# Kernel tuning notes

Hardware: AMD Instinct MI355X
Metric: run time of the kernel (lower is better)

The kernel has to match this reference:

```python
import jax, jax.numpy as jnp
import numpy as np

B, S, H = 2, 2048, 2048
NH, NKV = 16, 4
HD = H // NH          # 128
N_REP = NH // NKV     # 4


def _rotate_half(x):
    x1, x2 = x[..., : x.shape[-1] // 2], x[..., x.shape[-1] // 2 :]
    return jnp.concatenate((-x2, x1), axis=-1)


def setup_inputs() -> dict:
    key = jax.random.key(0)
    ks = jax.random.split(key, 5)
    hidden_states = jax.random.normal(ks[0], (B, S, H), dtype=jnp.float32)
    # true rotary tables [max_seq_len, head_dim]
    inv_freq = 1.0 / (10000.0 ** (np.arange(0, HD, 2, dtype=np.float32) / HD))
    t = np.arange(S, dtype=np.float32)
    freqs = np.outer(t, inv_freq)                    # [S, HD/2]
    emb = np.concatenate([freqs, freqs], axis=-1)    # [S, HD]
    cos = jnp.asarray(np.cos(emb))
    sin = jnp.asarray(np.sin(emb))
    Wq = jax.random.normal(ks[1], (H, NH * HD), dtype=jnp.float32) * 0.02
    Wk = jax.random.normal(ks[2], (H, NKV * HD), dtype=jnp.float32) * 0.02
    Wv = jax.random.normal(ks[3], (H, NKV * HD), dtype=jnp.float32) * 0.02
    Wo = jax.random.normal(ks[4], (NH * HD, H), dtype=jnp.float32) * 0.02
    attention_mask = jnp.ones((B, S), dtype=jnp.float32)  # 1 = keep
    return {"hidden_states": hidden_states, "cos": cos, "sin": sin,
            "Wq": Wq, "Wk": Wk, "Wv": Wv, "Wo": Wo,
            "attention_mask": attention_mask}


def reference(hidden_states, cos, sin, Wq, Wk, Wv, Wo, attention_mask):
    # Decoder self-attention: is_causal=True, use_rope=True, no cache, eval (dropout off).
    x = hidden_states
    b, s, _ = x.shape
    q = jnp.einsum('bsh,hd->bsd', x, Wq).reshape(b, s, NH, HD).transpose(0, 2, 1, 3)   # [b,nh,s,hd]
    k = jnp.einsum('bsh,hd->bsd', x, Wk).reshape(b, s, NKV, HD)
    v = jnp.einsum('bsh,hd->bsd', x, Wv).reshape(b, s, NKV, HD)
    # GQA repeat_kv: each kv head repeated n_rep times contiguously
    k = jnp.repeat(k, N_REP, axis=2).transpose(0, 2, 1, 3)   # [b,nh,s,hd]
    v = jnp.repeat(v, N_REP, axis=2).transpose(0, 2, 1, 3)
    # RoPE
    c = cos[:s][None, None, :, :]
    sn = sin[:s][None, None, :, :]
    q = q * c + _rotate_half(q) * sn
    k = k * c + _rotate_half(k) * sn
    # attention scores
    scores = jnp.einsum('bhqd,bhkd->bhqk', q, k) / jnp.sqrt(jnp.float32(HD))
    neg_inf = jnp.finfo(scores.dtype).min
    causal = jnp.triu(jnp.full((s, s), neg_inf, dtype=scores.dtype), k=1)
    scores = scores + causal[None, None, :, :]
    pad = (1.0 - attention_mask[:, None, None, :].astype(scores.dtype)) * neg_inf
    scores = scores + pad
    attn = jax.nn.softmax(scores.astype(jnp.float32), axis=-1).astype(q.dtype)
    out = jnp.einsum('bhqk,bhkd->bhqd', attn, v)             # [b,nh,s,hd]
    out = out.transpose(0, 2, 1, 3).reshape(b, s, NH * HD)
    return jnp.einsum('bsd,dh->bsh', out, Wo)
```

## Files before the change

kernel.cpp:

```cpp
#include <hip/hip_runtime.h>
#include <hip/hip_bf16.h>


typedef __bf16 bf16;
typedef __bf16 bf16x8 __attribute__((ext_vector_type(8)));
typedef __bf16 bf16x4 __attribute__((ext_vector_type(4)));
typedef float  f32x4  __attribute__((ext_vector_type(4)));
typedef float  f32x16 __attribute__((ext_vector_type(16)));

#define MFMA_BF16(a, b, c) __builtin_amdgcn_mfma_f32_16x16x32_bf16((a), (b), (c), 0, 0, 0)
#define MFMA32(a, b, c)    __builtin_amdgcn_mfma_f32_32x32x16_bf16((a), (b), (c), 0, 0, 0)

__device__ __forceinline__ void glds16(const bf16* g, char* l) {
  __builtin_amdgcn_global_load_lds((__attribute__((address_space(1))) const void*)g,
                                   (__attribute__((address_space(3))) void*)l, 16, 0, 0);
}

__global__ __launch_bounds__(256) void k_cvt_bf16(const float* __restrict__ in,
                                                  bf16* __restrict__ out, int n4) {
  int i = blockIdx.x * 256 + threadIdx.x;
  if (i < n4) {
    float4 v = ((const float4*)in)[i];
    bf16x4 o;
    o[0] = (bf16)v.x; o[1] = (bf16)v.y; o[2] = (bf16)v.z; o[3] = (bf16)v.w;
    ((bf16x4*)out)[i] = o;
  }
}

__global__ __launch_bounds__(256) void k_transpose_w4(const float* __restrict__ Wq,
                                                      const float* __restrict__ Wk,
                                                      const float* __restrict__ Wv,
                                                      const float* __restrict__ Wo,
                                                      bf16* __restrict__ Wtq,
                                                      bf16* __restrict__ Wtk,
                                                      bf16* __restrict__ Wtv,
                                                      bf16* __restrict__ Wto) {
  int z = blockIdx.z;
  const float* W; bf16* Wt; int N;
  if (z == 0)      { W = Wq; Wt = Wtq; N = 2048; }
  else if (z == 1) { W = Wo; Wt = Wto; N = 2048; }
  else if (z == 2) { W = Wk; Wt = Wtk; N = 512; }
  else             { W = Wv; Wt = Wtv; N = 512; }
  int nb = blockIdx.y * 32;
  if (nb >= N) return;
  __shared__ float tile[32][33];
  int tx = threadIdx.x, ty = threadIdx.y;
  int kb = blockIdx.x * 32;
#pragma unroll
  for (int i = 0; i < 4; ++i)
    tile[ty + i * 8][tx] = W[(size_t)(kb + ty + i * 8) * N + nb + tx];
  __syncthreads();
#pragma unroll
  for (int i = 0; i < 4; ++i)
    Wt[(size_t)(nb + ty + i * 8) * 2048 + kb + tx] = (bf16)tile[tx][ty + i * 8];
}

template <typename OUT>
__device__ void gemm_block(const bf16* __restrict__ A, const bf16* __restrict__ Bt,
                           OUT* __restrict__ C, int K, int ldc,
                           int rbase, int cbase, char* sm,
                           float rope_scl, const float* __restrict__ cosb,
                           const float* __restrict__ sinb,
                           bf16* __restrict__ vtr, int vkv) {
  const int tid = threadIdx.x;
  const int lane = tid & 63, wid = tid >> 6;
  const int l15 = lane & 15, lg = lane >> 4;
  char* Asm = sm;
  char* Bsm = sm + 32768;

  f32x4 acc[2][8];
#pragma unroll
  for (int i = 0; i < 2; ++i)
#pragma unroll
    for (int j = 0; j < 8; ++j)
#pragma unroll
      for (int r = 0; r < 4; ++r) acc[i][j][r] = 0.0f;

  const int ob = wid * 4096 + lane * 16;
  auto stage = [&](int buf, int kb) {
#pragma unroll
    for (int c = 0; c < 4; ++c) {
      int o = ob + c * 1024;
      int r = o >> 7;
      int cc = ((o >> 4) & 7) ^ (r & 7);
      int dst = wid * 4096 + c * 1024 + buf * 16384;
      glds16(A + (size_t)(rbase + r) * K + kb + cc * 8, Asm + dst);
      glds16(Bt + (size_t)(cbase + r) * K + kb + cc * 8, Bsm + dst);
    }
  };

  stage(0, 0);
  __syncthreads();
  const int nk = K >> 6;
  for (int t = 0; t < nk; ++t) {
    if (t + 1 < nk) stage((t + 1) & 1, (t + 1) << 6);
    const char* At  = Asm + (t & 1) * 16384;
    const char* Bti = Bsm + (t & 1) * 16384;
#pragma unroll
    for (int ks = 0; ks < 2; ++ks) {
      bf16x8 a[2], b[8];
#pragma unroll
      for (int rf = 0; rf < 2; ++rf) {
        int r = wid * 32 + rf * 16 + l15;
        int slot = (ks * 4 + lg) ^ (r & 7);
        a[rf] = *(const bf16x8*)(At + r * 128 + slot * 16);
      }
#pragma unroll
      for (int nf = 0; nf < 8; ++nf) {
        int n = nf * 16 + l15;
        int slot = (ks * 4 + lg) ^ (n & 7);
        b[nf] = *(const bf16x8*)(Bti + n * 128 + slot * 16);
      }
#pragma unroll
      for (int rf = 0; rf < 2; ++rf)
#pragma unroll
        for (int nf = 0; nf < 8; ++nf)
          acc[rf][nf] = MFMA_BF16(a[rf], b[nf], acc[rf][nf]);
    }
    __syncthreads();
  }

  if (rope_scl != 0.0f) {
#pragma unroll
    for (int rf = 0; rf < 2; ++rf)
#pragma unroll
      for (int r = 0; r < 4; ++r) {
        int s = (rbase + wid * 32 + rf * 16 + lg * 4 + r) & 2047;
#pragma unroll
        for (int nf = 0; nf < 4; ++nf) {
          int d = nf * 16 + l15;
          float v0 = acc[rf][nf][r], v1 = acc[rf][nf + 4][r];
          float c0 = cosb[s * 128 + d],      c1 = cosb[s * 128 + d + 64];
          float s0 = sinb[s * 128 + d],      s1 = sinb[s * 128 + d + 64];
          acc[rf][nf][r]     = (v0 * c0 - v1 * s0) * rope_scl;
          acc[rf][nf + 4][r] = (v1 * c1 + v0 * s1) * rope_scl;
        }
      }
  }

  if (vtr != nullptr) {
#pragma unroll
    for (int rf = 0; rf < 2; ++rf)
#pragma unroll
      for (int nf = 0; nf < 8; ++nf) {
        int s0 = wid * 32 + rf * 16 + lg * 4;
        int d = nf * 16 + l15;
        bf16x4 pk;
#pragma unroll
        for (int r = 0; r < 4; ++r) pk[r] = (bf16)acc[rf][nf][r];
        *(bf16x4*)(sm + d * 256 + ((s0 * 2) ^ ((d & 15) << 4))) = pk;
      }
    __syncthreads();
    const int b4 = (rbase >> 11) * 4;
    const int scol = rbase & 2047;
    const int so = tid & 15;
#pragma unroll
    for (int i = 0; i < 8; ++i) {
      int d = (tid >> 4) + i * 16;
      bf16x8 v = *(const bf16x8*)(sm + d * 256 + ((so * 16) ^ ((d & 15) << 4)));
      *(bf16x8*)(vtr + (size_t)((b4 + vkv) * 128 + d) * 2048 + scol + so * 8) = v;
    }
    return;
  }

#pragma unroll
  for (int rf = 0; rf < 2; ++rf)
#pragma unroll
    for (int nf = 0; nf < 8; ++nf)
#pragma unroll
      for (int r = 0; r < 4; ++r) {
        int row = rbase + wid * 32 + rf * 16 + lg * 4 + r;
        int col = cbase + nf * 16 + l15;
        C[(size_t)row * ldc + col] = (OUT)acc[rf][nf][r];
      }
}

__global__ __launch_bounds__(256, 2) void k_gemm_qkv(const bf16* __restrict__ X,
                                                     const bf16* __restrict__ Wtq,
                                                     const bf16* __restrict__ Wtk,
                                                     const bf16* __restrict__ Wtv,
                                                     bf16* __restrict__ Q,
                                                     bf16* __restrict__ Ko,
                                                     bf16* __restrict__ Vt,
                                                     const float* __restrict__ cosb,
                                                     const float* __restrict__ sinb,
                                                     float sclq) {
  __shared__ alignas(16) char sm[65536];
  int nb = blockIdx.y;
  int rbase = blockIdx.x * 128;
  if (nb < 16) {
    gemm_block<bf16>(X, Wtq, Q, 2048, 2048, rbase, nb * 128, sm, sclq, cosb, sinb,
                     nullptr, 0);
  } else if (nb < 20) {
    gemm_block<bf16>(X, Wtk, Ko, 2048, 512, rbase, (nb - 16) * 128, sm, 1.0f, cosb, sinb,
                     nullptr, 0);
  } else {
    gemm_block<bf16>(X, Wtv, (bf16*)nullptr, 2048, 512, rbase, (nb - 20) * 128, sm,
                     0.0f, nullptr, nullptr, Vt, nb - 20);
  }
}

__global__ __launch_bounds__(256, 2) void k_gemm_o(const bf16* __restrict__ AO,
                                                   const bf16* __restrict__ Wto,
                                                   float* __restrict__ Out) {
  __shared__ alignas(16) char sm[65536];
  gemm_block<float>(AO, Wto, Out, 2048, 2048, blockIdx.x * 128, blockIdx.y * 128, sm,
                    0.0f, nullptr, nullptr, nullptr, 0);
}

__global__ __launch_bounds__(256, 2) void k_fattn(const bf16* __restrict__ Qg,
                                                  const bf16* __restrict__ Kg,
                                                  const bf16* __restrict__ Vtg,
                                                  bf16* __restrict__ AO) {
  __shared__ alignas(16) char sm[65536];
  const int lane = threadIdx.x & 63, wid = threadIdx.x >> 6;
  const int l31 = lane & 31, lh = lane >> 5;
  const int wg = blockIdx.x;
  const int grp = wg & 7;
  const int b = grp >> 2, kv = grp & 3;
  const int inner = wg >> 3;
  const int head = kv * 4 + (inner & 3);
  const int strip = 15 - (inner >> 2);
  const int q0w = strip * 128 + wid * 32;
  const int nt = 2 * (strip + 1);

  const bf16 *ks[4], *vs[4];
#pragma unroll
  for (int i = 0; i < 4; ++i) {
    int c = wid * 256 + i * 64 + lane;
    int kr = c >> 4, kcc = (c & 15) ^ (kr & 15);
    ks[i] = Kg + (size_t)(b * 2048 + kr) * 512 + kv * 128 + kcc * 8;
    int vr = c >> 3, vcc = (c & 7) ^ (vr & 7);
    vs[i] = Vtg + (size_t)((b * 4 + kv) * 128 + vr) * 2048 + vcc * 8;
  }
  auto stage = [&](int t) {
    if (t >= nt) return;
    int kb = t << 6;
    char* base = sm + (t & 1) * 32768 + wid * 4096;
#pragma unroll
    for (int i = 0; i < 4; ++i) {
      glds16(ks[i] + (size_t)kb * 512, base + i * 1024);
      glds16(vs[i] + kb, base + 16384 + i * 1024);
    }
  };

  bf16x8 qf[8];
#pragma unroll
  for (int st = 0; st < 8; ++st)
    qf[st] = *(const bf16x8*)(Qg + (size_t)(b * 2048 + q0w + l31) * 2048 +
                              head * 128 + st * 16 + lh * 8);

  f32x16 o[4];
#pragma unroll
  for (int j = 0; j < 4; ++j)
#pragma unroll
    for (int r = 0; r < 16; ++r) o[j][r] = 0.0f;
  float mrun = -3e38f, lrun = 0.0f;

  stage(0);
  __syncthreads();

  for (int t = 0; t < nt; ++t) {
    const int kb = t << 6;
    stage(t + 1);
    const char* Kt = sm + (t & 1) * 32768;
    const char* Vt = Kt + 16384;

    if (kb <= q0w + 31) {
      f32x16 sa[2];
#pragma unroll
      for (int j = 0; j < 2; ++j)
#pragma unroll
        for (int r = 0; r < 16; ++r) sa[j][r] = 0.0f;
      __builtin_amdgcn_s_setprio(1);
#pragma unroll
      for (int st = 0; st < 8; ++st) {
#pragma unroll
        for (int kt = 0; kt < 2; ++kt) {
          int row = kt * 32 + l31;
          int slot = (st * 2 + lh) ^ (row & 15);
          bf16x8 ka = *(const bf16x8*)(Kt + row * 256 + slot * 16);
          sa[kt] = MFMA32(ka, qf[st], sa[kt]);
        }
      }
      __builtin_amdgcn_s_setprio(0);

      if (kb + 63 > q0w) {
        const int qi = q0w + l31;
#pragma unroll
        for (int kt = 0; kt < 2; ++kt)
#pragma unroll
          for (int r = 0; r < 16; ++r) {
            int kg = kb + kt * 32 + (r & 3) + 8 * (r >> 2) + 4 * lh;
            if (kg > qi) sa[kt][r] = -3e38f;
          }
      }

      float mx = sa[0][0];
#pragma unroll
      for (int kt = 0; kt < 2; ++kt)
#pragma unroll
        for (int r = 0; r < 16; ++r) mx = fmaxf(mx, sa[kt][r]);
      mx = fmaxf(mx, __shfl_xor(mx, 32));
      if (!__all(mx - mrun <= 8.0f)) {
        float mnew = fmaxf(mrun, mx);
        float fac = __builtin_amdgcn_exp2f(mrun - mnew);
        lrun *= fac;
#pragma unroll
        for (int j = 0; j < 4; ++j)
#pragma unroll
          for (int r = 0; r < 16; ++r) o[j][r] *= fac;
        mrun = mnew;
      }

      union UV { uint32_t u[4]; bf16x8 v; } frag[4];
      float rs = 0.0f;
#pragma unroll
      for (int kt = 0; kt < 2; ++kt) {
        float pe[16];
#pragma unroll
        for (int r = 0; r < 16; ++r) {
          pe[r] = __builtin_amdgcn_exp2f(sa[kt][r] - mrun);
          rs += pe[r];
        }
        uint32_t c[8];
#pragma unroll
        for (int g = 0; g < 8; ++g)
          asm("v_cvt_pk_bf16_f32 %0, %1, %2" : "=v"(c[g]) : "v"(pe[2 * g]), "v"(pe[2 * g + 1]));
#pragma unroll
        for (int f = 0; f < 2; ++f) {
          int bi = f * 4;
          uint32_t va = lh ? c[bi + 0] : c[bi + 2];
          uint32_t ra = (uint32_t)__shfl_xor((int)va, 32);
          uint32_t vb = lh ? c[bi + 1] : c[bi + 3];
          uint32_t rb = (uint32_t)__shfl_xor((int)vb, 32);
          UV& fr = frag[kt * 2 + f];
          fr.u[0] = lh ? ra : c[bi + 0];
          fr.u[1] = lh ? rb : c[bi + 1];
          fr.u[2] = lh ? c[bi + 2] : ra;
          fr.u[3] = lh ? c[bi + 3] : rb;
        }
      }
      rs += __shfl_xor(rs, 32);
      lrun += rs;

      __builtin_amdgcn_s_setprio(1);
#pragma unroll
      for (int dt = 0; dt < 4; ++dt) {
        int row = dt * 32 + l31;
#pragma unroll
        for (int kf = 0; kf < 4; ++kf) {
          int slot = (kf * 2 + lh) ^ (row & 7);
          bf16x8 va = *(const bf16x8*)(Vt + row * 128 + slot * 16);
          o[dt] = MFMA32(va, frag[kf].v, o[dt]);
        }
      }
      __builtin_amdgcn_s_setprio(0);
    }
    __syncthreads();
  }

  float linv = 1.0f / lrun;
  bf16* aop = AO + (size_t)(b * 2048 + q0w + l31) * 2048 + head * 128;
#pragma unroll
  for (int dt = 0; dt < 4; ++dt)
#pragma unroll
    for (int g = 0; g < 4; ++g) {
      bf16x4 pk;
#pragma unroll
      for (int j = 0; j < 4; ++j) pk[j] = (bf16)(o[dt][4 * g + j] * linv);
      *(bf16x4*)(aop + dt * 32 + g * 8 + lh * 4) = pk;
    }
}

extern "C" void kernel_launch(void* const* d_in, const int* in_sizes, int n_in,
                              void* d_out, int out_size, void* d_ws, size_t ws_size,
                              hipStream_t stream) {
  const float* hs   = (const float*)d_in[0];
  const float* cosb = (const float*)d_in[1];
  const float* sinb = (const float*)d_in[2];
  const float* Wq   = (const float*)d_in[3];
  const float* Wk   = (const float*)d_in[4];
  const float* Wv   = (const float*)d_in[5];
  const float* Wo   = (const float*)d_in[6];
  float* Out = (float*)d_out;

  char* ws = (char*)d_ws;
  size_t off = 0;
  auto alloc = [&](size_t bytes) { char* p = ws + off; off += bytes; return p; };
  bf16* Xbf = (bf16*)alloc((size_t)4096 * 2048 * 2);
  bf16* Wtq = (bf16*)alloc((size_t)2048 * 2048 * 2);
  bf16* Wtk = (bf16*)alloc((size_t)512 * 2048 * 2);
  bf16* Wtv = (bf16*)alloc((size_t)512 * 2048 * 2);
  bf16* Wto = (bf16*)alloc((size_t)2048 * 2048 * 2);
  bf16* Qb  = (bf16*)alloc((size_t)4096 * 2048 * 2);
  bf16* Kb  = (bf16*)alloc((size_t)4096 * 512 * 2);
  bf16* Vtb = (bf16*)alloc((size_t)4096 * 512 * 2);
  bf16* AO  = (bf16*)alloc((size_t)4096 * 2048 * 2);

  const float SCLQ = 0.08838834764831845f * 1.4426950408889634f;

  dim3 tb(32, 8);
  k_cvt_bf16<<<8192, 256, 0, stream>>>(hs, Xbf, 2097152);
  k_transpose_w4<<<dim3(64, 64, 4), tb, 0, stream>>>(Wq, Wk, Wv, Wo, Wtq, Wtk, Wtv, Wto);
  k_gemm_qkv<<<dim3(32, 24), 256, 0, stream>>>(Xbf, Wtq, Wtk, Wtv, Qb, Kb, Vtb,
                                               cosb, sinb, SCLQ);
  k_fattn<<<512, 256, 0, stream>>>(Qb, Kb, Vtb, AO);
  k_gemm_o<<<dim3(32, 16), 256, 0, stream>>>(AO, Wto, Out);
}
```

Measured before the change: 200.5 us.

## Fuse output projection into attention kernel via per-strip completion flags

Merges the attention and output-projection kernels into one persistent-style launch. Each attention block bumps a per-(batch,strip) counter when it finishes, then pulls O-projection tiles from a global atomic work queue and spin-waits until the matching attention strip is complete. This lets the O-GEMM overlap the tail of the causal attention and saves a launch. The cvt and transpose prep kernels are also merged into one launch. The cost is a memset plus atomic and spin-wait synchronisation, and forward progress relies on the attention blocks being resident or scheduled ahead of waiting blocks.

```diff
diff --git a/kernel.cpp b/kernel.cpp
--- a/kernel.cpp
+++ b/kernel.cpp
@@ -16,36 +16,34 @@
                                    (__attribute__((address_space(3))) void*)l, 16, 0, 0);
 }
 
-__global__ __launch_bounds__(256) void k_cvt_bf16(const float* __restrict__ in,
-                                                  bf16* __restrict__ out, int n4) {
-  int i = blockIdx.x * 256 + threadIdx.x;
-  if (i < n4) {
-    float4 v = ((const float4*)in)[i];
+__global__ __launch_bounds__(256) void k_prep(const float* __restrict__ hs,
+                                              bf16* __restrict__ Xbf,
+                                              const float* __restrict__ Wq,
+                                              const float* __restrict__ Wk,
+                                              const float* __restrict__ Wv,
+                                              const float* __restrict__ Wo,
+                                              bf16* __restrict__ Wtq,
+                                              bf16* __restrict__ Wtk,
+                                              bf16* __restrict__ Wtv,
+                                              bf16* __restrict__ Wto) {
+  int blk = blockIdx.x;
+  if (blk < 8192) {
+    int i = blk * 256 + threadIdx.x;
+    float4 v = ((const float4*)hs)[i];
     bf16x4 o;
     o[0] = (bf16)v.x; o[1] = (bf16)v.y; o[2] = (bf16)v.z; o[3] = (bf16)v.w;
-    ((bf16x4*)out)[i] = o;
-  }
-}
-
-__global__ __launch_bounds__(256) void k_transpose_w4(const float* __restrict__ Wq,
-                                                      const float* __restrict__ Wk,
-                                                      const float* __restrict__ Wv,
-                                                      const float* __restrict__ Wo,
-                                                      bf16* __restrict__ Wtq,
-                                                      bf16* __restrict__ Wtk,
-                                                      bf16* __restrict__ Wtv,
-                                                      bf16* __restrict__ Wto) {
-  int z = blockIdx.z;
+    ((bf16x4*)Xbf)[i] = o;
+    return;
+  }
+  int local = blk - 8192;
   const float* W; bf16* Wt; int N;
-  if (z == 0)      { W = Wq; Wt = Wtq; N = 2048; }
-  else if (z == 1) { W = Wo; Wt = Wto; N = 2048; }
-  else if (z == 2) { W = Wk; Wt = Wtk; N = 512; }
-  else             { W = Wv; Wt = Wtv; N = 512; }
-  int nb = blockIdx.y * 32;
-  if (nb >= N) return;
+  if (local < 4096)       { W = Wq; Wt = Wtq; N = 2048; }
+  else if (local < 8192)  { W = Wo; Wt = Wto; N = 2048; local -= 4096; }
+  else if (local < 9216)  { W = Wk; Wt = Wtk; N = 512;  local -= 8192; }
+  else                    { W = Wv; Wt = Wtv; N = 512;  local -= 9216; }
+  int kb = (local & 63) * 32, nb = (local >> 6) * 32;
   __shared__ float tile[32][33];
-  int tx = threadIdx.x, ty = threadIdx.y;
-  int kb = blockIdx.x * 32;
+  int tx = threadIdx.x & 31, ty = threadIdx.x >> 5;
 #pragma unroll
   for (int i = 0; i < 4; ++i)
     tile[ty + i * 8][tx] = W[(size_t)(kb + ty + i * 8) * N + nb + tx];
@@ -200,19 +198,15 @@
   }
 }
 
-__global__ __launch_bounds__(256, 2) void k_gemm_o(const bf16* __restrict__ AO,
-                                                   const bf16* __restrict__ Wto,
-                                                   float* __restrict__ Out) {
+__global__ __launch_bounds__(256, 2) void k_fattn_oproj(const bf16* __restrict__ Qg,
+                                                        const bf16* __restrict__ Kg,
+                                                        const bf16* __restrict__ Vtg,
+                                                        bf16* __restrict__ AO,
+                                                        const bf16* __restrict__ Wto,
+                                                        float* __restrict__ Out,
+                                                        uint32_t* __restrict__ flags) {
   __shared__ alignas(16) char sm[65536];
-  gemm_block<float>(AO, Wto, Out, 2048, 2048, blockIdx.x * 128, blockIdx.y * 128, sm,
-                    0.0f, nullptr, nullptr, nullptr, 0);
-}
-
-__global__ __launch_bounds__(256, 2) void k_fattn(const bf16* __restrict__ Qg,
-                                                  const bf16* __restrict__ Kg,
-                                                  const bf16* __restrict__ Vtg,
-                                                  bf16* __restrict__ AO) {
-  __shared__ alignas(16) char sm[65536];
+  __shared__ int smq;
   const int lane = threadIdx.x & 63, wid = threadIdx.x >> 6;
   const int l31 = lane & 31, lh = lane >> 5;
   const int wg = blockIdx.x;
@@ -224,153 +218,181 @@
   const int q0w = strip * 128 + wid * 32;
   const int nt = 2 * (strip + 1);
 
-  const bf16 *ks[4], *vs[4];
-#pragma unroll
-  for (int i = 0; i < 4; ++i) {
-    int c = wid * 256 + i * 64 + lane;
-    int kr = c >> 4, kcc = (c & 15) ^ (kr & 15);
-    ks[i] = Kg + (size_t)(b * 2048 + kr) * 512 + kv * 128 + kcc * 8;
-    int vr = c >> 3, vcc = (c & 7) ^ (vr & 7);
-    vs[i] = Vtg + (size_t)((b * 4 + kv) * 128 + vr) * 2048 + vcc * 8;
-  }
-  auto stage = [&](int t) {
-    if (t >= nt) return;
-    int kb = t << 6;
-    char* base = sm + (t & 1) * 32768 + wid * 4096;
+  {
+    const bf16 *ks[4], *vs[4];
 #pragma unroll
     for (int i = 0; i < 4; ++i) {
-      glds16(ks[i] + (size_t)kb * 512, base + i * 1024);
-      glds16(vs[i] + kb, base + 16384 + i * 1024);
-    }
-  };
-
-  bf16x8 qf[8];
-#pragma unroll
-  for (int st = 0; st < 8; ++st)
-    qf[st] = *(const bf16x8*)(Qg + (size_t)(b * 2048 + q0w + l31) * 2048 +
-                              head * 128 + st * 16 + lh * 8);
-
-  f32x16 o[4];
-#pragma unroll
-  for (int j = 0; j < 4; ++j)
-#pragma unroll
-    for (int r = 0; r < 16; ++r) o[j][r] = 0.0f;
-  float mrun = -3e38f, lrun = 0.0f;
-
-  stage(0);
-  __syncthreads();
-
-  for (int t = 0; t < nt; ++t) {
-    const int kb = t << 6;
-    stage(t + 1);
-    const char* Kt = sm + (t & 1) * 32768;
-    const char* Vt = Kt + 16384;
-
-    if (kb <= q0w + 31) {
-      f32x16 sa[2];
-#pragma unroll
-      for (int j = 0; j < 2; ++j)
-#pragma unroll
-        for (int r = 0; r < 16; ++r) sa[j][r] = 0.0f;
-      __builtin_amdgcn_s_setprio(1);
-#pragma unroll
-      for (int st = 0; st < 8; ++st) {
+      int c = wid * 256 + i * 64 + lane;
+      int kr = c >> 4, kcc = (c & 15) ^ (kr & 15);
+      ks[i] = Kg + (size_t)(b * 2048 + kr) * 512 + kv * 128 + kcc * 8;
+      int vr = c >> 3, vcc = (c & 7) ^ (vr & 7);
+      vs[i] = Vtg + (size_t)((b * 4 + kv) * 128 + vr) * 2048 + vcc * 8;
+    }
+    auto stage = [&](int t) {
+      if (t >= nt) return;
+      int kb = t << 6;
+      char* base = sm + (t & 1) * 32768 + wid * 4096;
+#pragma unroll
+      for (int i = 0; i < 4; ++i) {
+        glds16(ks[i] + (size_t)kb * 512, base + i * 1024);
+        glds16(vs[i] + kb, base + 16384 + i * 1024);
+      }
+    };
+
+    bf16x8 qf[8];
+#pragma unroll
+    for (int st = 0; st < 8; ++st)
+      qf[st] = *(const bf16x8*)(Qg + (size_t)(b * 2048 + q0w + l31) * 2048 +
+                                head * 128 + st * 16 + lh * 8);
+
+    f32x16 o[4];
+#pragma unroll
+    for (int j = 0; j < 4; ++j)
+#pragma unroll
+      for (int r = 0; r < 16; ++r) o[j][r] = 0.0f;
+    float mrun = -3e38f, lrun = 0.0f;
+
+    stage(0);
+    __syncthreads();
+
+    for (int t = 0; t < nt; ++t) {
+      const int kb = t << 6;
+      stage(t + 1);
+      const char* Kt = sm + (t & 1) * 32768;
+      const char* Vt = Kt + 16384;
+
+      if (kb <= q0w + 31) {
+        f32x16 sa[2];
+#pragma unroll
+        for (int j = 0; j < 2; ++j)
+#pragma unroll
+          for (int r = 0; r < 16; ++r) sa[j][r] = 0.0f;
+        __builtin_amdgcn_s_setprio(1);
+#pragma unroll
+        for (int st = 0; st < 8; ++st) {
+#pragma unroll
+          for (int kt = 0; kt < 2; ++kt) {
+            int row = kt * 32 + l31;
+            int slot = (st * 2 + lh) ^ (row & 15);
+            bf16x8 ka = *(const bf16x8*)(Kt + row * 256 + slot * 16);
+            sa[kt] = MFMA32(ka, qf[st], sa[kt]);
+          }
+        }
+        __builtin_amdgcn_s_setprio(0);
+
+        if (kb + 63 > q0w) {
+          const int qi = q0w + l31;
+#pragma unroll
+          for (int kt = 0; kt < 2; ++kt)
+#pragma unroll
+            for (int r = 0; r < 16; ++r) {
+              int kg = kb + kt * 32 + (r & 3) + 8 * (r >> 2) + 4 * lh;
+              if (kg > qi) sa[kt][r] = -3e38f;
+            }
+        }
+
+        float mx = sa[0][0];
+#pragma unroll
+        for (int kt = 0; kt < 2; ++kt)
+#pragma unroll
+          for (int r = 0; r < 16; ++r) mx = fmaxf(mx, sa[kt][r]);
+        mx = fmaxf(mx, __shfl_xor(mx, 32));
+        if (!__all(mx - mrun <= 8.0f)) {
+          float mnew = fmaxf(mrun, mx);
+          float fac = __builtin_amdgcn_exp2f(mrun - mnew);
+          lrun *= fac;
+#pragma unroll
+          for (int j = 0; j < 4; ++j)
+#pragma unroll
+            for (int r = 0; r < 16; ++r) o[j][r] *= fac;
+          mrun = mnew;
+        }
+
+        union UV { uint32_t u[4]; bf16x8 v; } frag[4];
+        float rs = 0.0f;
 #pragma unroll
         for (int kt = 0; kt < 2; ++kt) {
-          int row = kt * 32 + l31;
-          int slot = (st * 2 + lh) ^ (row & 15);
-          bf16x8 ka = *(const bf16x8*)(Kt + row * 256 + slot * 16);
-          sa[kt] = MFMA32(ka, qf[st], sa[kt]);
-        }
-      }
-      __builtin_amdgcn_s_setprio(0);
-
-      if (kb + 63 > q0w) {
-        const int qi = q0w + l31;
-#pragma unroll
-        for (int kt = 0; kt < 2; ++kt)
+          float pe[16];
 #pragma unroll
           for (int r = 0; r < 16; ++r) {
-            int kg = kb + kt * 32 + (r & 3) + 8 * (r >> 2) + 4 * lh;
-            if (kg > qi) sa[kt][r] = -3e38f;
+            pe[r] = __builtin_amdgcn_exp2f(sa[kt][r] - mrun);
+            rs += pe[r];
           }
-      }
-
-      float mx = sa[0][0];
-#pragma unroll
-      for (int kt = 0; kt < 2; ++kt)
-#pragma unroll
-        for (int r = 0; r < 16; ++r) mx = fmaxf(mx, sa[kt][r]);
-      mx = fmaxf(mx, __shfl_xor(mx, 32));
-      if (!__all(mx - mrun <= 8.0f)) {
-        float mnew = fmaxf(mrun, mx);
-        float fac = __builtin_amdgcn_exp2f(mrun - mnew);
-        lrun *= fac;
-#pragma unroll
-        for (int j = 0; j < 4; ++j)
-#pragma unroll
-          for (int r = 0; r < 16; ++r) o[j][r] *= fac;
-        mrun = mnew;
-      }
-
-      union UV { uint32_t u[4]; bf16x8 v; } frag[4];
-      float rs = 0.0f;
-#pragma unroll
-      for (int kt = 0; kt < 2; ++kt) {
-        float pe[16];
-#pragma unroll
-        for (int r = 0; r < 16; ++r) {
-          pe[r] = __builtin_amdgcn_exp2f(sa[kt][r] - mrun);
-          rs += pe[r];
-        }
-        uint32_t c[8];
-#pragma unroll
-        for (int g = 0; g < 8; ++g)
-          asm("v_cvt_pk_bf16_f32 %0, %1, %2" : "=v"(c[g]) : "v"(pe[2 * g]), "v"(pe[2 * g + 1]));
-#pragma unroll
-        for (int f = 0; f < 2; ++f) {
-          int bi = f * 4;
-          uint32_t va = lh ? c[bi + 0] : c[bi + 2];
-          uint32_t ra = (uint32_t)__shfl_xor((int)va, 32);
-          uint32_t vb = lh ? c[bi + 1] : c[bi + 3];
-          uint32_t rb = (uint32_t)__shfl_xor((int)vb, 32);
-          UV& fr = frag[kt * 2 + f];
-          fr.u[0] = lh ? ra : c[bi + 0];
-          fr.u[1] = lh ? rb : c[bi + 1];
-          fr.u[2] = lh ? c[bi + 2] : ra;
-          fr.u[3] = lh ? c[bi + 3] : rb;
-        }
-      }
-      rs += __shfl_xor(rs, 32);
-      lrun += rs;
-
-      __builtin_amdgcn_s_setprio(1);
-#pragma unroll
-      for (int dt = 0; dt < 4; ++dt) {
-        int row = dt * 32 + l31;
-#pragma unroll
-        for (int kf = 0; kf < 4; ++kf) {
-          int slot = (kf * 2 + lh) ^ (row & 7);
-          bf16x8 va = *(const bf16x8*)(Vt + row * 128 + slot * 16);
-          o[dt] = MFMA32(va, frag[kf].v, o[dt]);
-        }
-      }
-      __builtin_amdgcn_s_setprio(0);
-    }
-    __syncthreads();
-  }
-
-  float linv = 1.0f / lrun;
-  bf16* aop = AO + (size_t)(b * 2048 + q0w + l31) * 2048 + head * 128;
-#pragma unroll
-  for (int dt = 0; dt < 4; ++dt)
-#pragma unroll
-    for (int g = 0; g < 4; ++g) {
-      bf16x4 pk;
-#pragma unroll
-      for (int j = 0; j < 4; ++j) pk[j] = (bf16)(o[dt][4 * g + j] * linv);
-      *(bf16x4*)(aop + dt * 32 + g * 8 + lh * 4) = pk;
-    }
+          uint32_t c[8];
+#pragma unroll
+          for (int g = 0; g < 8; ++g)
+            asm("v_cvt_pk_bf16_f32 %0, %1, %2" : "=v"(c[g]) : "v"(pe[2 * g]), "v"(pe[2 * g + 1]));
+#pragma unroll
+          for (int f = 0; f < 2; ++f) {
+            int bi = f * 4;
+            uint32_t va = lh ? c[bi + 0] : c[bi + 2];
+            uint32_t ra = (uint32_t)__shfl_xor((int)va, 32);
+            uint32_t vb = lh ? c[bi + 1] : c[bi + 3];
+            uint32_t rb = (uint32_t)__shfl_xor((int)vb, 32);
+            UV& fr = frag[kt * 2 + f];
+            fr.u[0] = lh ? ra : c[bi + 0];
+            fr.u[1] = lh ? rb : c[bi + 1];
+            fr.u[2] = lh ? c[bi + 2] : ra;
+            fr.u[3] = lh ? c[bi + 3] : rb;
+          }
+        }
+        rs += __shfl_xor(rs, 32);
+        lrun += rs;
+
+        __builtin_amdgcn_s_setprio(1);
+#pragma unroll
+        for (int dt = 0; dt < 4; ++dt) {
+          int row = dt * 32 + l31;
+#pragma unroll
+          for (int kf = 0; kf < 4; ++kf) {
+            int slot = (kf * 2 + lh) ^ (row & 7);
+            bf16x8 va = *(const bf16x8*)(Vt + row * 128 + slot * 16);
+            o[dt] = MFMA32(va, frag[kf].v, o[dt]);
+          }
+        }
+        __builtin_amdgcn_s_setprio(0);
+      }
+      __syncthreads();
+    }
+
+    float linv = 1.0f / lrun;
+    bf16* aop = AO + (size_t)(b * 2048 + q0w + l31) * 2048 + head * 128;
+#pragma unroll
+    for (int dt = 0; dt < 4; ++dt)
+#pragma unroll
+      for (int g = 0; g < 4; ++g) {
+        bf16x4 pk;
+#pragma unroll
+        for (int j = 0; j < 4; ++j) pk[j] = (bf16)(o[dt][4 * g + j] * linv);
+        *(bf16x4*)(aop + dt * 32 + g * 8 + lh * 4) = pk;
+      }
+  }
+
+  __threadfence();
+  if (threadIdx.x == 0)
+    __hip_atomic_fetch_add(&flags[b * 16 + strip], 1u, __ATOMIC_RELEASE,
+                           __HIP_MEMORY_SCOPE_AGENT);
+
+  for (;;) {
+    if (threadIdx.x == 0)
+      smq = (int)__hip_atomic_fetch_add(&flags[32], 1u, __ATOMIC_RELAXED,
+                                        __HIP_MEMORY_SCOPE_AGENT);
+    __syncthreads();
+    int q = smq;
+    __syncthreads();
+    if (q >= 512) break;
+    int ostrip = q >> 5, ob = (q >> 4) & 1, ocol = q & 15;
+    if (threadIdx.x == 0) {
+      while (__hip_atomic_load(&flags[ob * 16 + ostrip], __ATOMIC_ACQUIRE,
+                               __HIP_MEMORY_SCOPE_AGENT) < 16u)
+        __builtin_amdgcn_s_sleep(8);
+    }
+    __syncthreads();
+    __threadfence();
+    gemm_block<float>(AO, Wto, Out, 2048, 2048, ob * 2048 + ostrip * 128,
+                      ocol * 128, sm, 0.0f, nullptr, nullptr, nullptr, 0);
+    __syncthreads();
+  }
 }
 
 extern "C" void kernel_launch(void* const* d_in, const int* in_sizes, int n_in,
@@ -397,14 +419,13 @@
   bf16* Kb  = (bf16*)alloc((size_t)4096 * 512 * 2);
   bf16* Vtb = (bf16*)alloc((size_t)4096 * 512 * 2);
   bf16* AO  = (bf16*)alloc((size_t)4096 * 2048 * 2);
+  uint32_t* flags = (uint32_t*)alloc(256);
 
   const float SCLQ = 0.08838834764831845f * 1.4426950408889634f;
 
-  dim3 tb(32, 8);
-  k_cvt_bf16<<<8192, 256, 0, stream>>>(hs, Xbf, 2097152);
-  k_transpose_w4<<<dim3(64, 64, 4), tb, 0, stream>>>(Wq, Wk, Wv, Wo, Wtq, Wtk, Wtv, Wto);
+  hipMemsetAsync(flags, 0, 256, stream);
+  k_prep<<<18432, 256, 0, stream>>>(hs, Xbf, Wq, Wk, Wv, Wo, Wtq, Wtk, Wtv, Wto);
   k_gemm_qkv<<<dim3(32, 24), 256, 0, stream>>>(Xbf, Wtq, Wtk, Wtv, Qb, Kb, Vtb,
                                                cosb, sinb, SCLQ);
-  k_fattn<<<512, 256, 0, stream>>>(Qb, Kb, Vtb, AO);
-  k_gemm_o<<<dim3(32, 16), 256, 0, stream>>>(AO, Wto, Out);
-}
+  k_fattn_oproj<<<512, 256, 0, stream>>>(Qb, Kb, Vtb, AO, Wto, Out, flags);
+}
```

New measurement: 352.3 us. 75.7% more time.
